# Kernel optimization log

Measured on AMD Instinct MI355X. Metric: run time of the kernel, lower is better.

Reference implementation:

```python
import jax, jax.numpy as jnp
import numpy as np

NUM_HEADS = 32
NUM_KV_HEADS = 8
HEAD_DIM = 128
QUERY_SCALAR = 128.0
SOFTCAP = 50.0
SEQ = 2048
MIN_ATTN_SCORE = -1e9


def setup_inputs() -> dict:
    key = jax.random.key(0)
    k1, k2, k3 = jax.random.split(key, 3)
    B = 2
    Q = jax.random.normal(k1, (B, NUM_HEADS, SEQ, HEAD_DIM), dtype=jnp.float32)
    K = jax.random.normal(k2, (B, NUM_KV_HEADS, SEQ, HEAD_DIM), dtype=jnp.float32)
    V = jax.random.normal(k3, (B, NUM_KV_HEADS, SEQ, HEAD_DIM), dtype=jnp.float32)
    # additive causal mask: 0 on/below diagonal, -1e9 strictly above (torch.triu(full, diagonal=1))
    causal_mask = jnp.triu(jnp.full((SEQ, SEQ), MIN_ATTN_SCORE, dtype=jnp.float32), k=1)
    return {"Q": Q, "K": K, "V": V, "causal_mask": causal_mask}


def reference(Q, K, V, causal_mask):
    B, H, q_len, d = Q.shape
    kv_len = K.shape[2]
    g = H // NUM_KV_HEADS  # GQA group size
    scale = QUERY_SCALAR ** (-0.5)
    # group query heads instead of materializing expanded K/V
    Qg = (Q * scale).reshape(B, NUM_KV_HEADS, g, q_len, d)
    # scores [B, kv_heads, g, q, kv]
    A = jnp.einsum('bkgqd,bkld->bkgql', Qg, K)
    A = SOFTCAP * jnp.tanh(A * (1.0 / SOFTCAP))
    A = A + causal_mask[:q_len, :kv_len]
    A = jax.nn.softmax(A.astype(jnp.float32), axis=-1).astype(Q.dtype)
    O = jnp.einsum('bkgql,bkld->bkgqd', A, V)           # [B, kvH, g, q, d]
    O = O.reshape(B, H, q_len, d).transpose(0, 2, 1, 3)  # [B, q, H, d]
    return O.reshape(B, q_len, H * d)
```

## Files before the change

### kernel.cpp

```cpp
#include <hip/hip_runtime.h>
#include <hip/hip_bf16.h>


constexpr int S_LEN = 2048;
constexpr int HD    = 128;
constexpr int NH    = 32;
constexpr int NKV   = 8;
constexpr int BQ    = 128;
constexpr int BK    = 64;
constexpr int QT    = S_LEN / BQ;
constexpr int NT64  = S_LEN / BK;

constexpr int KS_OFF = 0;
constexpr int VT_OFF = 16384;
constexpr int PS_OFF = 32768;
constexpr int SMEM_BYTES = 51200;

using bf16x8 = __attribute__((ext_vector_type(8))) short;
using f32x4  = __attribute__((ext_vector_type(4))) float;

__device__ __forceinline__ unsigned short f2bf(float f) {
    unsigned int u = __float_as_uint(f);
    u += 0x7FFFu + ((u >> 16) & 1u);
    return (unsigned short)(u >> 16);
}
__device__ __forceinline__ unsigned pack2bf(float a, float b) {
    union { __hip_bfloat162 h; unsigned u; } cv;
    cv.h = __float22bfloat162_rn(float2{a, b});
    return cv.u;
}
__device__ __forceinline__ void gld_lds16(const void* g, void* l) {
    __builtin_amdgcn_global_load_lds(
        (const __attribute__((address_space(1))) unsigned int*)g,
        (__attribute__((address_space(3))) unsigned int*)l, 16, 0, 0);
}

__global__ __launch_bounds__(256) void cvt_k(const float* __restrict__ in,
                                             unsigned short* __restrict__ out) {
    const size_t i0 = ((size_t)blockIdx.x * 256 + threadIdx.x) * 8;
    float4 a = *(const float4*)(in + i0);
    float4 b = *(const float4*)(in + i0 + 4);
    ushort4 lo, hi;
    lo.x = f2bf(a.x); lo.y = f2bf(a.y); lo.z = f2bf(a.z); lo.w = f2bf(a.w);
    hi.x = f2bf(b.x); hi.y = f2bf(b.y); hi.z = f2bf(b.z); hi.w = f2bf(b.w);
    *(ushort4*)(out + i0)     = lo;
    *(ushort4*)(out + i0 + 4) = hi;
}

__global__ __launch_bounds__(256) void cvt_v(const float* __restrict__ in,
                                             unsigned short* __restrict__ out) {
    const int kt = blockIdx.x, kh = blockIdx.y, b = blockIdx.z;
    const float* src = in + (((size_t)b * NKV + kh) * S_LEN + (size_t)kt * BK) * HD;
    unsigned short* dst = out + ((size_t)(b * NKV + kh) * NT64 + kt) * (size_t)HD * BK;

    __shared__ __align__(16) float Vs[BK * (HD + 4)];
    const int t = threadIdx.x;
    #pragma unroll
    for (int i = 0; i < 8; ++i) {
        int f = t + i * 256;
        int row = f >> 5, c4 = (f & 31) << 2;
        *(float4*)&Vs[row * (HD + 4) + c4] = *(const float4*)(src + row * HD + c4);
    }
    __syncthreads();
    const int d = t >> 1, half = t & 1;
    unsigned wbuf[16];
    #pragma unroll
    for (int m = 0; m < 16; ++m) {
        int p0 = 32 * half + 2 * m;
        int k0 = 16 * (p0 & 3) + (p0 >> 2);
        wbuf[m] = pack2bf(Vs[k0 * (HD + 4) + d], Vs[(k0 + 16) * (HD + 4) + d]);
    }
    unsigned short* o = dst + d * BK + 32 * half;
    #pragma unroll
    for (int m = 0; m < 4; ++m)
        *(uint4*)(o + 8 * m) = make_uint4(wbuf[4*m], wbuf[4*m+1], wbuf[4*m+2], wbuf[4*m+3]);
}

template <bool PRE>
__global__ __launch_bounds__(256, 3) void fa_fwd(
    const float* __restrict__ Q, const float* __restrict__ Kf,
    const float* __restrict__ Vf, const unsigned short* __restrict__ Kb,
    const unsigned short* __restrict__ Vb, float* __restrict__ Out)
{
    const int qt = (QT - 1) - blockIdx.z;
    const int h  = blockIdx.x;
    const int b  = blockIdx.y;
    const int kh = h >> 2;

    __shared__ __align__(16) char smem[SMEM_BYTES];
    unsigned short* Ks = (unsigned short*)(smem + KS_OFF);
    unsigned short* Vt = (unsigned short*)(smem + VT_OFF);
    unsigned short* Ps = (unsigned short*)(smem + PS_OFF);

    const int t    = threadIdx.x;
    const int lane = t & 63;
    const int w    = t >> 6;
    const int l15  = lane & 15;
    const int quad = lane >> 4;

    const float* Qb = Q + (((size_t)b * NH + h) * S_LEN + (size_t)qt * BQ) * HD;
    const float scale = 0.08838834764831845f;

    bf16x8 qf[2][4];
    #pragma unroll
    for (int mt = 0; mt < 2; ++mt) {
        const float* qp = Qb + (size_t)(32*w + 16*mt + l15) * HD + 8*quad;
        #pragma unroll
        for (int ks = 0; ks < 4; ++ks) {
            float4 a = *(const float4*)(qp + 32*ks);
            float4 c = *(const float4*)(qp + 32*ks + 4);
            bf16x8 f;
            f[0] = (short)f2bf(a.x*scale); f[1] = (short)f2bf(a.y*scale);
            f[2] = (short)f2bf(a.z*scale); f[3] = (short)f2bf(a.w*scale);
            f[4] = (short)f2bf(c.x*scale); f[5] = (short)f2bf(c.y*scale);
            f[6] = (short)f2bf(c.z*scale); f[7] = (short)f2bf(c.w*scale);
            qf[mt][ks] = f;
        }
    }

    f32x4 o[2][8];
    #pragma unroll
    for (int mt = 0; mt < 2; ++mt)
        #pragma unroll
        for (int nt = 0; nt < 8; ++nt)
            #pragma unroll
            for (int r = 0; r < 4; ++r) o[mt][nt][r] = 0.0f;

    float lpart[2][4];
    #pragma unroll
    for (int mt = 0; mt < 2; ++mt)
        #pragma unroll
        for (int r = 0; r < 4; ++r) lpart[mt][r] = 0.0f;

    const unsigned short* Kp = Kb + ((size_t)b * NKV + kh) * (size_t)S_LEN * HD;
    const unsigned short* Vp = Vb + ((size_t)b * NKV + kh) * (size_t)NT64 * HD * BK;
    const float* Kf0 = Kf + ((size_t)b * NKV + kh) * (size_t)S_LEN * HD;
    const float* Vf0 = Vf + ((size_t)b * NKV + kh) * (size_t)S_LEN * HD;

    int koff[4], kl[4], voff[4], vl[4];
    if constexpr (PRE) {
        #pragma unroll
        for (int c = 0; c < 4; ++c) {
            int rk  = 4*c + (lane >> 4);
            koff[c] = (16*w + rk) * 256 + 16 * ((lane & 15) ^ (rk & 7));
            kl[c]   = (16*w + 4*c) * 256;
            int rv  = 8*c + (lane >> 3);
            voff[c] = (32*w + rv) * 128 + 16 * ((lane & 7) ^ ((lane >> 3) & 7));
            vl[c]   = (32*w + 8*c) * 128;
        }
    }

    const int n_kt = 2 * (qt + 1);
    for (int kt = 0; kt < n_kt; ++kt) {
        if constexpr (PRE) {
            const char* kg = (const char*)Kp + (size_t)kt * (BK * HD * 2);
            const char* vg = (const char*)Vp + (size_t)kt * (HD * BK * 2);
            __syncthreads();
            #pragma unroll
            for (int c = 0; c < 4; ++c) {
                gld_lds16(kg + koff[c], (char*)Ks + kl[c]);
                gld_lds16(vg + voff[c], (char*)Vt + vl[c]);
            }
            __syncthreads();
        } else {
            const float* kg = Kf0 + (size_t)(kt * BK) * HD;
            const float* vg = Vf0 + (size_t)(kt * BK) * HD;
            float4 ka[4][2]; float va[4][8];
            #pragma unroll
            for (int c = 0; c < 4; ++c) {
                int f = 256*c + t;
                int row = f >> 4, ch = f & 15, chg = (f & 15) ^ ((f >> 4) & 7);
                (void)ch;
                ka[c][0] = *(const float4*)(kg + row * HD + 8*chg);
                ka[c][1] = *(const float4*)(kg + row * HD + 8*chg + 4);
                int rv = f >> 3, cvg = (f & 7) ^ ((f >> 3) & 7);
                #pragma unroll
                for (int j = 0; j < 8; ++j) {
                    int p = 8*cvg + j;
                    int k = 16*(p & 3) + (p >> 2);
                    va[c][j] = vg[(size_t)k * HD + rv];
                }
            }
            __syncthreads();
            #pragma unroll
            for (int c = 0; c < 4; ++c) {
                int f = 256*c + t;
                int row = f >> 4, ch = f & 15;
                bf16x8 kk;
                kk[0]=(short)f2bf(ka[c][0].x); kk[1]=(short)f2bf(ka[c][0].y);
                kk[2]=(short)f2bf(ka[c][0].z); kk[3]=(short)f2bf(ka[c][0].w);
                kk[4]=(short)f2bf(ka[c][1].x); kk[5]=(short)f2bf(ka[c][1].y);
                kk[6]=(short)f2bf(ka[c][1].z); kk[7]=(short)f2bf(ka[c][1].w);
                *(bf16x8*)((char*)Ks + row * 256 + 16 * ch) = kk;
                int rv = f >> 3, cv = f & 7;
                bf16x8 vv;
                #pragma unroll
                for (int j = 0; j < 8; ++j) vv[j] = (short)f2bf(va[c][j]);
                *(bf16x8*)((char*)Vt + rv * 128 + 16 * cv) = vv;
            }
            __syncthreads();
        }

        f32x4 s[2][4];
        #pragma unroll
        for (int mt = 0; mt < 2; ++mt)
            #pragma unroll
            for (int nt = 0; nt < 4; ++nt)
                #pragma unroll
                for (int r = 0; r < 4; ++r) s[mt][nt][r] = 0.0f;
        #pragma unroll
        for (int ks = 0; ks < 4; ++ks) {
            bf16x8 kf[4];
            #pragma unroll
            for (int nt = 0; nt < 4; ++nt)
                kf[nt] = *(const bf16x8*)((const char*)Ks + (16*nt + l15) * 256
                                          + 16 * ((4*ks + quad) ^ (l15 & 7)));
            #pragma unroll
            for (int nt = 0; nt < 4; ++nt) {
                s[0][nt] = __builtin_amdgcn_mfma_f32_16x16x32_bf16(qf[0][ks], kf[nt], s[0][nt], 0, 0, 0);
                s[1][nt] = __builtin_amdgcn_mfma_f32_16x16x32_bf16(qf[1][ks], kf[nt], s[1][nt], 0, 0, 0);
            }
        }

        const bool diag = (kt >= 2 * qt);
        #pragma unroll
        for (int mt = 0; mt < 2; ++mt) {
            #pragma unroll
            for (int r = 0; r < 4; ++r) {
                float x[4];
                #pragma unroll
                for (int nt = 0; nt < 4; ++nt) {
                    float v  = s[mt][nt][r];
                    float v2 = v * v;
                    float fcap = __builtin_fmaf(v2, __builtin_fmaf(v2, 2.13333333e-8f, -1.33333333e-4f), 1.0f);
                    x[nt] = (v * 1.44269504f) * fcap;
                }
                if (diag) {
                    const int qrow = qt * BQ + 32*w + 16*mt + 4*quad + r;
                    #pragma unroll
                    for (int nt = 0; nt < 4; ++nt)
                        if (kt * BK + 16*nt + l15 > qrow) x[nt] = -1e30f;
                }
                float p0 = __builtin_amdgcn_exp2f(x[0]);
                float p1 = __builtin_amdgcn_exp2f(x[1]);
                float p2 = __builtin_amdgcn_exp2f(x[2]);
                float p3 = __builtin_amdgcn_exp2f(x[3]);
                lpart[mt][r] += (p0 + p1) + (p2 + p3);
                uint2 pw; pw.x = pack2bf(p0, p1); pw.y = pack2bf(p2, p3);
                *(uint2*)((char*)Ps + (32*w + 16*mt + 4*quad + r) * 144 + 8 * l15) = pw;
            }
        }

        __syncthreads();

        #pragma unroll
        for (int ks = 0; ks < 2; ++ks) {
            bf16x8 pf[2];
            #pragma unroll
            for (int mt = 0; mt < 2; ++mt)
                pf[mt] = *(const bf16x8*)((const char*)Ps + (32*w + 16*mt + l15) * 144
                                          + 64*ks + 16*quad);
            #pragma unroll
            for (int nt = 0; nt < 8; ++nt) {
                bf16x8 vf = *(const bf16x8*)((const char*)Vt + (16*nt + l15) * 128
                                             + 16 * ((4*ks + quad) ^ (l15 & 7)));
                o[0][nt] = __builtin_amdgcn_mfma_f32_16x16x32_bf16(pf[0], vf, o[0][nt], 0, 0, 0);
                o[1][nt] = __builtin_amdgcn_mfma_f32_16x16x32_bf16(pf[1], vf, o[1][nt], 0, 0, 0);
            }
        }
    }

    float inv[2][4];
    #pragma unroll
    for (int mt = 0; mt < 2; ++mt) {
        #pragma unroll
        for (int r = 0; r < 4; ++r) {
            float l = lpart[mt][r];
            l += __shfl_xor(l, 1);
            l += __shfl_xor(l, 2);
            l += __shfl_xor(l, 4);
            l += __shfl_xor(l, 8);
            inv[mt][r] = 1.0f / l;
        }
    }
    float* sc = (float*)smem;
    const int tw = t & 31;
    #pragma unroll
    for (int p = 0; p < 2; ++p) {
        __syncthreads();
        #pragma unroll
        for (int r = 0; r < 4; ++r) {
            const int sr = 16*w + 4*quad + r;
            #pragma unroll
            for (int nt = 0; nt < 8; ++nt)
                sc[sr * 132 + 16*nt + l15] = o[p][nt][r] * inv[p][r];
        }
        __syncthreads();
        #pragma unroll
        for (int it = 0; it < 8; ++it) {
            const int sr = (t >> 5) + 8 * it;
            float4 v = *(const float4*)&sc[sr * 132 + 4 * tw];
            const int ql = 32 * (sr >> 4) + 16 * p + (sr & 15);
            float* op = Out + ((size_t)b * S_LEN + (size_t)qt * BQ + ql) * (size_t)(NH * HD)
                        + (size_t)h * HD + 4 * tw;
            *(float4*)op = v;
        }
    }
}

extern "C" void kernel_launch(void* const* d_in, const int* in_sizes, int n_in,
                              void* d_out, int out_size, void* d_ws, size_t ws_size,
                              hipStream_t stream) {
    const float* Q = (const float*)d_in[0];
    const float* K = (const float*)d_in[1];
    const float* V = (const float*)d_in[2];
    float* Out = (float*)d_out;

    const size_t kv_elems = (size_t)2 * NKV * S_LEN * HD;
    const size_t need     = 2 * kv_elems * sizeof(unsigned short);

    dim3 grid(NH, 2, QT);
    if (ws_size >= need) {
        unsigned short* Kb = (unsigned short*)d_ws;
        unsigned short* Vb = Kb + kv_elems;
        cvt_k<<<dim3((unsigned)(kv_elems / (256 * 8))), dim3(256), 0, stream>>>(K, Kb);
        cvt_v<<<dim3(NT64, NKV, 2), dim3(256), 0, stream>>>(V, Vb);
        fa_fwd<true><<<grid, dim3(256), 0, stream>>>(Q, K, V, Kb, Vb, Out);
    } else {
        fa_fwd<false><<<grid, dim3(256), 0, stream>>>(Q, K, V, nullptr, nullptr, Out);
    }
}
```

Measured before the change: 272.0 us.

## Compute transposed S=K·Qᵀ so P stays in registers, dropping LDS round-trip

Swaps the MFMA operand order for the score computation so each lane holds a column of scores that maps directly onto the A-operand layout of the P·V MFMA. The probabilities are packed to bf16 in registers, which removes the P staging buffer in shared memory, a barrier per KV tile, and the LDS writes and reads. The V pre-transpose permutation and the fp32 V load path are rewritten to match the new k ordering. The row-sum reduction changes to cross-quad shuffles plus a final lane gather, and the tanh polynomial folds in log2(e). Shared memory use drops, which could raise occupancy, at the cost of more intricate index mapping that is easy to get wrong.

Result: faster. 239.3 us (-12.0%).

```diff
diff --git a/kernel.cpp b/kernel.cpp
--- a/kernel.cpp
+++ b/kernel.cpp
@@ -13,8 +13,7 @@
 
 constexpr int KS_OFF = 0;
 constexpr int VT_OFF = 16384;
-constexpr int PS_OFF = 32768;
-constexpr int SMEM_BYTES = 51200;
+constexpr int SMEM_BYTES = 33792;
 
 using bf16x8 = __attribute__((ext_vector_type(8))) short;
 using f32x4  = __attribute__((ext_vector_type(4))) float;
@@ -66,9 +65,9 @@
     unsigned wbuf[16];
     #pragma unroll
     for (int m = 0; m < 16; ++m) {
-        int p0 = 32 * half + 2 * m;
-        int k0 = 16 * (p0 & 3) + (p0 >> 2);
-        wbuf[m] = pack2bf(Vs[k0 * (HD + 4) + d], Vs[(k0 + 16) * (HD + 4) + d]);
+        int k0 = 32 * half + 16 * ((m >> 1) & 1) + 8 * ((m >> 3) & 1)
+               + 4 * ((m >> 2) & 1) + 2 * (m & 1);
+        wbuf[m] = pack2bf(Vs[k0 * (HD + 4) + d], Vs[(k0 + 1) * (HD + 4) + d]);
     }
     unsigned short* o = dst + d * BK + 32 * half;
     #pragma unroll
@@ -90,7 +89,6 @@
     __shared__ __align__(16) char smem[SMEM_BYTES];
     unsigned short* Ks = (unsigned short*)(smem + KS_OFF);
     unsigned short* Vt = (unsigned short*)(smem + VT_OFF);
-    unsigned short* Ps = (unsigned short*)(smem + PS_OFF);
 
     const int t    = threadIdx.x;
     const int lane = t & 63;
@@ -126,11 +124,7 @@
             #pragma unroll
             for (int r = 0; r < 4; ++r) o[mt][nt][r] = 0.0f;
 
-    float lpart[2][4];
-    #pragma unroll
-    for (int mt = 0; mt < 2; ++mt)
-        #pragma unroll
-        for (int r = 0; r < 4; ++r) lpart[mt][r] = 0.0f;
+    float lpart[2] = {0.0f, 0.0f};
 
     const unsigned short* Kp = Kb + ((size_t)b * NKV + kh) * (size_t)S_LEN * HD;
     const unsigned short* Vp = Vb + ((size_t)b * NKV + kh) * (size_t)NT64 * HD * BK;
@@ -169,15 +163,15 @@
             #pragma unroll
             for (int c = 0; c < 4; ++c) {
                 int f = 256*c + t;
-                int row = f >> 4, ch = f & 15, chg = (f & 15) ^ ((f >> 4) & 7);
-                (void)ch;
+                int row = f >> 4, chg = (f & 15) ^ ((f >> 4) & 7);
                 ka[c][0] = *(const float4*)(kg + row * HD + 8*chg);
                 ka[c][1] = *(const float4*)(kg + row * HD + 8*chg + 4);
                 int rv = f >> 3, cvg = (f & 7) ^ ((f >> 3) & 7);
                 #pragma unroll
                 for (int j = 0; j < 8; ++j) {
                     int p = 8*cvg + j;
-                    int k = 16*(p & 3) + (p >> 2);
+                    int k = 32*((p >> 5) & 1) + 16*((p >> 2) & 1) + 8*((p >> 4) & 1)
+                          + 4*((p >> 3) & 1) + 2*((p >> 1) & 1) + (p & 1);
                     va[c][j] = vg[(size_t)k * HD + rv];
                 }
             }
@@ -201,13 +195,13 @@
             __syncthreads();
         }
 
-        f32x4 s[2][4];
-        #pragma unroll
-        for (int mt = 0; mt < 2; ++mt)
-            #pragma unroll
-            for (int nt = 0; nt < 4; ++nt)
+        f32x4 s[4][2];
+        #pragma unroll
+        for (int nt = 0; nt < 4; ++nt)
+            #pragma unroll
+            for (int mt = 0; mt < 2; ++mt)
                 #pragma unroll
-                for (int r = 0; r < 4; ++r) s[mt][nt][r] = 0.0f;
+                for (int r = 0; r < 4; ++r) s[nt][mt][r] = 0.0f;
         #pragma unroll
         for (int ks = 0; ks < 4; ++ks) {
             bf16x8 kf[4];
@@ -217,55 +211,49 @@
                                           + 16 * ((4*ks + quad) ^ (l15 & 7)));
             #pragma unroll
             for (int nt = 0; nt < 4; ++nt) {
-                s[0][nt] = __builtin_amdgcn_mfma_f32_16x16x32_bf16(qf[0][ks], kf[nt], s[0][nt], 0, 0, 0);
-                s[1][nt] = __builtin_amdgcn_mfma_f32_16x16x32_bf16(qf[1][ks], kf[nt], s[1][nt], 0, 0, 0);
-            }
-        }
-
-        const bool diag = (kt >= 2 * qt);
+                s[nt][0] = __builtin_amdgcn_mfma_f32_16x16x32_bf16(kf[nt], qf[0][ks], s[nt][0], 0, 0, 0);
+                s[nt][1] = __builtin_amdgcn_mfma_f32_16x16x32_bf16(kf[nt], qf[1][ks], s[nt][1], 0, 0, 0);
+            }
+        }
+
+        const bool diag  = (kt >= 2 * qt);
+        const int  kbase = kt * BK;
+        bf16x8 pf[2][2];
         #pragma unroll
         for (int mt = 0; mt < 2; ++mt) {
-            #pragma unroll
-            for (int r = 0; r < 4; ++r) {
-                float x[4];
+            const int qrow = qt * BQ + 32*w + 16*mt + l15;
+            #pragma unroll
+            for (int nt = 0; nt < 4; ++nt) {
                 #pragma unroll
-                for (int nt = 0; nt < 4; ++nt) {
-                    float v  = s[mt][nt][r];
+                for (int r = 0; r < 4; ++r) {
+                    float v  = s[nt][mt][r];
                     float v2 = v * v;
-                    float fcap = __builtin_fmaf(v2, __builtin_fmaf(v2, 2.13333333e-8f, -1.33333333e-4f), 1.0f);
-                    x[nt] = (v * 1.44269504f) * fcap;
+                    float fc = __builtin_fmaf(v2, __builtin_fmaf(v2, 3.07779053e-8f, -1.92359146e-4f), 1.44269504f);
+                    float x = v * fc;
+                    if (diag && (kbase + 16*nt + 4*quad + r > qrow)) x = -1e30f;
+                    s[nt][mt][r] = __builtin_amdgcn_exp2f(x);
                 }
-                if (diag) {
-                    const int qrow = qt * BQ + 32*w + 16*mt + 4*quad + r;
-                    #pragma unroll
-                    for (int nt = 0; nt < 4; ++nt)
-                        if (kt * BK + 16*nt + l15 > qrow) x[nt] = -1e30f;
-                }
-                float p0 = __builtin_amdgcn_exp2f(x[0]);
-                float p1 = __builtin_amdgcn_exp2f(x[1]);
-                float p2 = __builtin_amdgcn_exp2f(x[2]);
-                float p3 = __builtin_amdgcn_exp2f(x[3]);
-                lpart[mt][r] += (p0 + p1) + (p2 + p3);
-                uint2 pw; pw.x = pack2bf(p0, p1); pw.y = pack2bf(p2, p3);
-                *(uint2*)((char*)Ps + (32*w + 16*mt + 4*quad + r) * 144 + 8 * l15) = pw;
-            }
-        }
-
-        __syncthreads();
+                lpart[mt] += (s[nt][mt][0] + s[nt][mt][1]) + (s[nt][mt][2] + s[nt][mt][3]);
+            }
+            #pragma unroll
+            for (int ks = 0; ks < 2; ++ks) {
+                union { bf16x8 v; unsigned u[4]; } pk;
+                pk.u[0] = pack2bf(s[2*ks][mt][0],     s[2*ks][mt][1]);
+                pk.u[1] = pack2bf(s[2*ks][mt][2],     s[2*ks][mt][3]);
+                pk.u[2] = pack2bf(s[2*ks + 1][mt][0], s[2*ks + 1][mt][1]);
+                pk.u[3] = pack2bf(s[2*ks + 1][mt][2], s[2*ks + 1][mt][3]);
+                pf[mt][ks] = pk.v;
+            }
+        }
 
         #pragma unroll
         for (int ks = 0; ks < 2; ++ks) {
-            bf16x8 pf[2];
-            #pragma unroll
-            for (int mt = 0; mt < 2; ++mt)
-                pf[mt] = *(const bf16x8*)((const char*)Ps + (32*w + 16*mt + l15) * 144
-                                          + 64*ks + 16*quad);
             #pragma unroll
             for (int nt = 0; nt < 8; ++nt) {
                 bf16x8 vf = *(const bf16x8*)((const char*)Vt + (16*nt + l15) * 128
                                              + 16 * ((4*ks + quad) ^ (l15 & 7)));
-                o[0][nt] = __builtin_amdgcn_mfma_f32_16x16x32_bf16(pf[0], vf, o[0][nt], 0, 0, 0);
-                o[1][nt] = __builtin_amdgcn_mfma_f32_16x16x32_bf16(pf[1], vf, o[1][nt], 0, 0, 0);
+                o[0][nt] = __builtin_amdgcn_mfma_f32_16x16x32_bf16(pf[0][ks], vf, o[0][nt], 0, 0, 0);
+                o[1][nt] = __builtin_amdgcn_mfma_f32_16x16x32_bf16(pf[1][ks], vf, o[1][nt], 0, 0, 0);
             }
         }
     }
@@ -273,16 +261,14 @@
     float inv[2][4];
     #pragma unroll
     for (int mt = 0; mt < 2; ++mt) {
-        #pragma unroll
-        for (int r = 0; r < 4; ++r) {
-            float l = lpart[mt][r];
-            l += __shfl_xor(l, 1);
-            l += __shfl_xor(l, 2);
-            l += __shfl_xor(l, 4);
-            l += __shfl_xor(l, 8);
-            inv[mt][r] = 1.0f / l;
-        }
-    }
+        float L = lpart[mt];
+        L += __shfl_xor(L, 16);
+        L += __shfl_xor(L, 32);
+        #pragma unroll
+        for (int r = 0; r < 4; ++r)
+            inv[mt][r] = 1.0f / __shfl(L, 20*quad + r);
+    }
+
     float* sc = (float*)smem;
     const int tw = t & 31;
     #pragma unroll
```
